# Kernel tuning notes

Hardware: AMD Instinct MI355X
Metric: run time of the kernel (lower is better)

## Reference

```python
import jax, jax.numpy as jnp
import numpy as np

N = 50000   # nodes
E = 800000  # edges
F_IN, F_HID, F_CLS = 128, 128, 40


def gcn_conv(x, W, b, src, dst, dinv):
    # PyG GCNConv: h = x @ W; symmetric-normalized aggregation with self-loops; + bias
    h = x @ W
    coef = (dinv[src] * dinv[dst])[:, None]              # [E,1] edge norm
    agg = jax.ops.segment_sum(h[src] * coef, dst, num_segments=N)
    agg = agg + h * (dinv * dinv)[:, None]               # self-loop term (norm = 1/deg)
    return agg + b


def setup_inputs() -> dict:
    key = jax.random.key(0)
    ks = jax.random.split(key, 8)
    s = 0.06
    return {
        "x": jax.random.normal(ks[0], (N, F_IN), jnp.float32),
        "edge_index": jax.random.randint(ks[1], (2, E), 0, N, dtype=jnp.int64),
        "W1": jax.random.normal(ks[2], (F_IN, F_HID), jnp.float32) * s,
        "b1": jnp.zeros((F_HID,), jnp.float32),
        "W2": jax.random.normal(ks[3], (F_HID, F_HID), jnp.float32) * s,
        "b2": jnp.zeros((F_HID,), jnp.float32),
        "Wc": jax.random.normal(ks[4], (F_HID, F_CLS), jnp.float32) * s,
        "bc": jnp.zeros((F_CLS,), jnp.float32),
    }


def reference(x, edge_index, W1, b1, W2, b2, Wc, bc):
    src, dst = edge_index[0], edge_index[1]
    # degree incl. self-loop, counted at target nodes (PyG default)
    deg = jnp.zeros((N,), x.dtype).at[dst].add(1.0) + 1.0
    dinv = jax.lax.rsqrt(deg)
    h = jax.nn.relu(gcn_conv(x, W1, b1, src, dst, dinv))
    h = jax.nn.relu(gcn_conv(h, W2, b2, src, dst, dinv))
    return h @ Wc + bc
```

## Files before the change

kernel.cpp:

```cpp
#include <hip/hip_runtime.h>

#define FDIM 128
#define FCLS 40
#define EPB  2048
#define BSH  8
#define BKN  (1 << BSH)

typedef short s16x8 __attribute__((ext_vector_type(8)));
typedef float f32x4 __attribute__((ext_vector_type(4)));

__device__ __forceinline__ float bf2f(unsigned short u) {
    union { unsigned int i; float f; } v; v.i = ((unsigned int)u) << 16; return v.f;
}
__device__ __forceinline__ unsigned short f2bf(float f) {
    union { float f; unsigned int i; } v; v.f = f;
    unsigned int u = v.i + 0x7FFFu + ((v.i >> 16) & 1u);
    return (unsigned short)(u >> 16);
}

__global__ __launch_bounds__(256) void bin_hist(const int* __restrict__ dst,
                                                int* __restrict__ hist,
                                                int E, int nblkA, int NB) {
    __shared__ int h[BKN];
    int t = threadIdx.x;
    for (int i = t; i < BKN; i += 256) h[i] = 0;
    __syncthreads();
    int base = blockIdx.x * EPB;
    int end = min(base + EPB, E);
    for (int i = base + t; i < end; i += 256) atomicAdd(&h[dst[i] >> BSH], 1);
    __syncthreads();
    for (int i = t; i < NB; i += 256) hist[i * nblkA + blockIdx.x] = h[i];
}

__global__ __launch_bounds__(256) void hscan_partial(const int* __restrict__ data,
                                                     int* __restrict__ bsums, int n) {
    __shared__ int s[256];
    int t = threadIdx.x;
    int base = blockIdx.x * 1024 + t * 4;
    int v = 0;
#pragma unroll
    for (int j = 0; j < 4; ++j) if (base + j < n) v += data[base + j];
    s[t] = v;
    __syncthreads();
    for (int off = 128; off > 0; off >>= 1) {
        if (t < off) s[t] += s[t + off];
        __syncthreads();
    }
    if (t == 0) bsums[blockIdx.x] = s[0];
}

__global__ __launch_bounds__(256) void hscan_block(int* __restrict__ bsums, int nb) {
    __shared__ int s[256];
    int t = threadIdx.x;
    s[t] = (t < nb) ? bsums[t] : 0;
    __syncthreads();
    for (int off = 1; off < 256; off <<= 1) {
        int x = 0;
        if (t >= off) x = s[t - off];
        __syncthreads();
        s[t] += x;
        __syncthreads();
    }
    if (t < nb) bsums[t] = (t > 0) ? s[t - 1] : 0;
}

__global__ __launch_bounds__(256) void hscan_final(int* __restrict__ data,
                                                   const int* __restrict__ bsums, int n) {
    __shared__ int s[256];
    int t = threadIdx.x;
    int idx = blockIdx.x * 1024 + t * 4;
    int v[4];
    int sum = 0;
#pragma unroll
    for (int j = 0; j < 4; ++j) {
        v[j] = (idx + j < n) ? data[idx + j] : 0;
        sum += v[j];
    }
    s[t] = sum;
    __syncthreads();
    for (int off = 1; off < 256; off <<= 1) {
        int x = 0;
        if (t >= off) x = s[t - off];
        __syncthreads();
        s[t] += x;
        __syncthreads();
    }
    int running = bsums[blockIdx.x] + s[t] - sum;
#pragma unroll
    for (int j = 0; j < 4; ++j) {
        if (idx + j < n) data[idx + j] = running;
        running += v[j];
    }
}

__global__ __launch_bounds__(256) void bin_scatter(const int* __restrict__ src,
                                                   const int* __restrict__ dst,
                                                   const int* __restrict__ histS,
                                                   int2* __restrict__ binned,
                                                   int E, int nblkA, int NB) {
    __shared__ int cur[BKN];
    int t = threadIdx.x;
    for (int i = t; i < NB; i += 256) cur[i] = histS[i * nblkA + blockIdx.x];
    __syncthreads();
    int base = blockIdx.x * EPB;
    int end = min(base + EPB, E);
    for (int i = base + t; i < end; i += 256) {
        int d = dst[i];
        int pos = atomicAdd(&cur[d >> BSH], 1);
        binned[pos] = make_int2(src[i], d);
    }
}

__global__ __launch_bounds__(256) void node_hist_scan(const int2* __restrict__ binned,
                                                      const int* __restrict__ histS,
                                                      int* __restrict__ offsets,
                                                      float* __restrict__ dinv,
                                                      int N, int E, int nblkA, int NB) {
    int b = blockIdx.x;
    int node0 = b << BSH;
    int t = threadIdx.x;
    __shared__ int c[BKN];
    c[t] = 0;
    __syncthreads();
    int lo = histS[b * nblkA];
    int hi = (b == NB - 1) ? E : histS[(b + 1) * nblkA];
    for (int i = lo + t; i < hi; i += 256) {
        int2 p = binned[i];
        atomicAdd(&c[p.y - node0], 1);
    }
    __syncthreads();
    int v = c[t];
    for (int off = 1; off < 256; off <<= 1) {
        int x = (t >= off) ? c[t - off] : 0;
        __syncthreads();
        c[t] += x;
        __syncthreads();
    }
    int excl = lo + c[t] - v;
    int idx = node0 + t;
    if (idx < N) {
        offsets[idx] = excl;
        dinv[idx] = rsqrtf((float)v + 1.0f);
        if (idx == N - 1) offsets[N] = excl + v;
    }
}

__global__ __launch_bounds__(256) void csr_scatter(const int2* __restrict__ binned,
                                                   const int* __restrict__ offsets,
                                                   int* __restrict__ srcAdj, int N) {
    int b = blockIdx.x;
    int node0 = b << BSH;
    int node1 = min(node0 + BKN, N);
    __shared__ int cur[BKN];
    int t = threadIdx.x;
    if (node0 + t < node1) cur[t] = offsets[node0 + t];
    __syncthreads();
    int lo = offsets[node0];
    int hi = offsets[node1];
    for (int i = lo + t; i < hi; i += 256) {
        int2 p = binned[i];
        int pos = atomicAdd(&cur[p.y - node0], 1);
        srcAdj[pos] = p.x;
    }
}

__global__ __launch_bounds__(256) void pack_all(const float* __restrict__ W1,
                                                const float* __restrict__ W2,
                                                const float* __restrict__ Wc,
                                                unsigned short* __restrict__ Wp1,
                                                unsigned short* __restrict__ Wp2,
                                                unsigned short* __restrict__ Wpc) {
    int blk = blockIdx.x;
    const float* W; unsigned short* Wp; int ncols, ct;
    if (blk < 8)       { W = W1; Wp = Wp1; ncols = FDIM; ct = blk; }
    else if (blk < 16) { W = W2; Wp = Wp2; ncols = FDIM; ct = blk - 8; }
    else               { W = Wc; Wp = Wpc; ncols = FCLS; ct = blk - 16; }
    int t = ct * 256 + threadIdx.x;
    int lane = t & 63, ks = (t >> 6) & 3;
    int n  = ct * 16 + (lane & 15);
    int kb = ks * 32 + (lane >> 4) * 8;
    unsigned short v[8];
#pragma unroll
    for (int j = 0; j < 8; ++j) {
        v[j] = (n < ncols) ? f2bf(W[(size_t)(kb + j) * ncols + n]) : (unsigned short)0;
    }
    ushort4* o = (ushort4*)(Wp + (size_t)t * 8);
    o[0] = ushort4{v[0], v[1], v[2], v[3]};
    o[1] = ushort4{v[4], v[5], v[6], v[7]};
}

__global__ __launch_bounds__(256) void gemm_mfma_f32A(const float* __restrict__ A,
                                                      const unsigned short* __restrict__ Wp,
                                                      unsigned short* __restrict__ C, int M) {
    int wave = threadIdx.x >> 6;
    int lane = threadIdx.x & 63;
    int row0 = (blockIdx.x * 4 + wave) * 16;
    if (row0 >= M) return;
    int m = lane & 15;
    int g = lane >> 4;

    const float4* Arow = (const float4*)(A + (size_t)(row0 + m) * FDIM);
    s16x8 a[4];
#pragma unroll
    for (int ks = 0; ks < 4; ++ks) {
        float4 lo = Arow[ks * 8 + g * 2];
        float4 hi = Arow[ks * 8 + g * 2 + 1];
        s16x8 av;
        av[0] = (short)f2bf(lo.x); av[1] = (short)f2bf(lo.y);
        av[2] = (short)f2bf(lo.z); av[3] = (short)f2bf(lo.w);
        av[4] = (short)f2bf(hi.x); av[5] = (short)f2bf(hi.y);
        av[6] = (short)f2bf(hi.z); av[7] = (short)f2bf(hi.w);
        a[ks] = av;
    }

    for (int ct = 0; ct < 8; ++ct) {
        f32x4 acc = {0.f, 0.f, 0.f, 0.f};
#pragma unroll
        for (int ks = 0; ks < 4; ++ks) {
            s16x8 b = *(const s16x8*)(Wp + ((size_t)((ct * 4 + ks) * 64 + lane)) * 8);
            acc = __builtin_amdgcn_mfma_f32_16x16x32_bf16(a[ks], b, acc, 0, 0, 0);
        }
        int n  = ct * 16 + m;
        int r0 = row0 + g * 4;
#pragma unroll
        for (int r = 0; r < 4; ++r)
            C[(size_t)(r0 + r) * FDIM + n] = f2bf(acc[r]);
    }
}

__global__ __launch_bounds__(256) void gemm_mfma(const unsigned short* __restrict__ A,
                                                 const unsigned short* __restrict__ Wp,
                                                 unsigned short* __restrict__ C, int M) {
    int wave = threadIdx.x >> 6;
    int lane = threadIdx.x & 63;
    int row0 = (blockIdx.x * 4 + wave) * 16;
    if (row0 >= M) return;
    int m = lane & 15;
    int g = lane >> 4;

    const s16x8* Arow = (const s16x8*)(A + (size_t)(row0 + m) * FDIM);
    s16x8 a[4];
#pragma unroll
    for (int ks = 0; ks < 4; ++ks) a[ks] = Arow[ks * 4 + g];

    for (int ct = 0; ct < 8; ++ct) {
        f32x4 acc = {0.f, 0.f, 0.f, 0.f};
#pragma unroll
        for (int ks = 0; ks < 4; ++ks) {
            s16x8 b = *(const s16x8*)(Wp + ((size_t)((ct * 4 + ks) * 64 + lane)) * 8);
            acc = __builtin_amdgcn_mfma_f32_16x16x32_bf16(a[ks], b, acc, 0, 0, 0);
        }
        int n  = ct * 16 + m;
        int r0 = row0 + g * 4;
#pragma unroll
        for (int r = 0; r < 4; ++r)
            C[(size_t)(r0 + r) * FDIM + n] = f2bf(acc[r]);
    }
}

__global__ __launch_bounds__(256) void classifier_mfma(const unsigned short* __restrict__ A,
                                                       const unsigned short* __restrict__ Wp,
                                                       const float* __restrict__ bc,
                                                       float* __restrict__ out, int M) {
    int wave = threadIdx.x >> 6;
    int lane = threadIdx.x & 63;
    int row0 = (blockIdx.x * 4 + wave) * 16;
    if (row0 >= M) return;
    int m = lane & 15;
    int g = lane >> 4;

    const s16x8* Arow = (const s16x8*)(A + (size_t)(row0 + m) * FDIM);
    s16x8 a[4];
#pragma unroll
    for (int ks = 0; ks < 4; ++ks) a[ks] = Arow[ks * 4 + g];

    for (int ct = 0; ct < 3; ++ct) {
        f32x4 acc = {0.f, 0.f, 0.f, 0.f};
#pragma unroll
        for (int ks = 0; ks < 4; ++ks) {
            s16x8 b = *(const s16x8*)(Wp + ((size_t)((ct * 4 + ks) * 64 + lane)) * 8);
            acc = __builtin_amdgcn_mfma_f32_16x16x32_bf16(a[ks], b, acc, 0, 0, 0);
        }
        int n = ct * 16 + m;
        if (n < FCLS) {
            float bias = bc[n];
            int r0 = row0 + g * 4;
#pragma unroll
            for (int r = 0; r < 4; ++r)
                out[(size_t)(r0 + r) * FCLS + n] = acc[r] + bias;
        }
    }
}

__global__ __launch_bounds__(256) void agg_fused(const unsigned short* __restrict__ H,
                                                 const float* __restrict__ dinv,
                                                 const float* __restrict__ bias,
                                                 const int* __restrict__ srcAdj,
                                                 const int* __restrict__ offsets,
                                                 unsigned short* __restrict__ OUT, int N) {
    int node = blockIdx.x * 16 + (threadIdx.x >> 4);
    if (node >= N) return;
    int lane = threadIdx.x & 15;

    const s16x8* H8 = (const s16x8*)H;
    float di = dinv[node];
    float d2 = di * di;

    s16x8 h = H8[(size_t)node * 16 + lane];
    float acc[8];
#pragma unroll
    for (int j = 0; j < 8; ++j) acc[j] = bf2f((unsigned short)h[j]) * d2;

    int e   = offsets[node];
    int end = offsets[node + 1];
    for (; e + 4 <= end; e += 4) {
        int s0 = srcAdj[e + 0], s1 = srcAdj[e + 1];
        int s2 = srcAdj[e + 2], s3 = srcAdj[e + 3];
        float c0 = dinv[s0] * di, c1 = dinv[s1] * di;
        float c2 = dinv[s2] * di, c3 = dinv[s3] * di;
        s16x8 a0 = H8[(size_t)s0 * 16 + lane];
        s16x8 a1 = H8[(size_t)s1 * 16 + lane];
        s16x8 a2 = H8[(size_t)s2 * 16 + lane];
        s16x8 a3 = H8[(size_t)s3 * 16 + lane];
#pragma unroll
        for (int j = 0; j < 8; ++j) {
            acc[j] = fmaf(bf2f((unsigned short)a0[j]), c0, acc[j]);
            acc[j] = fmaf(bf2f((unsigned short)a1[j]), c1, acc[j]);
            acc[j] = fmaf(bf2f((unsigned short)a2[j]), c2, acc[j]);
            acc[j] = fmaf(bf2f((unsigned short)a3[j]), c3, acc[j]);
        }
    }
    for (; e < end; ++e) {
        int s0 = srcAdj[e];
        float c0 = dinv[s0] * di;
        s16x8 a0 = H8[(size_t)s0 * 16 + lane];
#pragma unroll
        for (int j = 0; j < 8; ++j)
            acc[j] = fmaf(bf2f((unsigned short)a0[j]), c0, acc[j]);
    }

    float4 b0 = ((const float4*)bias)[lane * 2];
    float4 b1 = ((const float4*)bias)[lane * 2 + 1];
    float bb[8] = {b0.x, b0.y, b0.z, b0.w, b1.x, b1.y, b1.z, b1.w};
    s16x8 o;
#pragma unroll
    for (int j = 0; j < 8; ++j)
        o[j] = (short)f2bf(fmaxf(acc[j] + bb[j], 0.0f));
    ((s16x8*)OUT)[(size_t)node * 16 + lane] = o;
}

extern "C" void kernel_launch(void* const* d_in, const int* in_sizes, int n_in,
                              void* d_out, int out_size, void* d_ws, size_t ws_size,
                              hipStream_t stream) {
    const float* x  = (const float*)d_in[0];
    const int*   ei = (const int*)d_in[1];
    const float* W1 = (const float*)d_in[2];
    const float* b1 = (const float*)d_in[3];
    const float* W2 = (const float*)d_in[4];
    const float* b2 = (const float*)d_in[5];
    const float* Wc = (const float*)d_in[6];
    const float* bc = (const float*)d_in[7];
    float* out = (float*)d_out;

    int N = in_sizes[0] / FDIM;
    int E = in_sizes[1] / 2;
    const int* src = ei;
    const int* dst = ei + E;

    int nblkA = (E + EPB - 1) / EPB;
    int NB    = (N + BKN - 1) >> BSH;
    int mfmaBlocks = (N / 16 + 3) / 4;
    int aggBlocks  = (N + 15) / 16;
    int histN = NB * nblkA;
    int hscanBlocks = (histN + 1023) / 1024;

    int2* binned   = (int2*)d_ws;
    int*  srcAdj   = (int*)(binned + E);
    int*  offsets  = srcAdj + E;
    int*  hist     = offsets + (N + 1);
    int*  bsums    = hist + histN;
    float* dinv    = (float*)(bsums + 256);
    unsigned short* Wp1 = (unsigned short*)(dinv + N);
    unsigned short* Wp2 = Wp1 + 8 * 4 * 64 * 8;
    unsigned short* Wpc = Wp2 + 8 * 4 * 64 * 8;
    unsigned short* Hbuf = Wpc + 3 * 4 * 64 * 8;
    unsigned short* Abuf = Hbuf + (size_t)N * FDIM;

    bin_hist<<<nblkA, 256, 0, stream>>>(dst, hist, E, nblkA, NB);
    hscan_partial<<<hscanBlocks, 256, 0, stream>>>(hist, bsums, histN);
    hscan_block<<<1, 256, 0, stream>>>(bsums, hscanBlocks);
    hscan_final<<<hscanBlocks, 256, 0, stream>>>(hist, bsums, histN);
    bin_scatter<<<nblkA, 256, 0, stream>>>(src, dst, hist, binned, E, nblkA, NB);
    node_hist_scan<<<NB, 256, 0, stream>>>(binned, hist, offsets, dinv, N, E, nblkA, NB);
    csr_scatter<<<NB, 256, 0, stream>>>(binned, offsets, srcAdj, N);

    pack_all<<<19, 256, 0, stream>>>(W1, W2, Wc, Wp1, Wp2, Wpc);

    gemm_mfma_f32A<<<mfmaBlocks, 256, 0, stream>>>(x, Wp1, Hbuf, N);
    agg_fused<<<aggBlocks, 256, 0, stream>>>(Hbuf, dinv, b1, srcAdj, offsets, Abuf, N);

    gemm_mfma<<<mfmaBlocks, 256, 0, stream>>>(Abuf, Wp2, Hbuf, N);
    agg_fused<<<aggBlocks, 256, 0, stream>>>(Hbuf, dinv, b2, srcAdj, offsets, Abuf, N);

    classifier_mfma<<<mfmaBlocks, 256, 0, stream>>>(Abuf, Wpc, bc, out, N);
}
```

Baseline: 158.4 us.

## Pack edge records, precompute fp16 edge coefficients, and split features into column quarters

The feature matrices move to a layout split into four 32-column quarters, and aggregation blocks each handle one quarter. Gathers then touch a 64-byte slice per node within a smaller working set, which should improve L2 hit rates. Edge records are packed into 32 bits (16-bit src and dst for binning; src plus an fp16 normalization coefficient for the CSR), which halves the bytes moved and removes the per-edge dinv lookups during aggregation. EPB also doubles. Packing node ids into 16 bits only works while N < 65536, so it relies on the test size, and the fp16 coefficients lose some precision.

```diff
diff --git a/kernel.cpp b/kernel.cpp
--- a/kernel.cpp
+++ b/kernel.cpp
@@ -1,8 +1,9 @@
 #include <hip/hip_runtime.h>
+#include <hip/hip_fp16.h>
 
 #define FDIM 128
 #define FCLS 40
-#define EPB  2048
+#define EPB  4096
 #define BSH  8
 #define BKN  (1 << BSH)
 
@@ -23,7 +24,7 @@
                                                 int E, int nblkA, int NB) {
     __shared__ int h[BKN];
     int t = threadIdx.x;
-    for (int i = t; i < BKN; i += 256) h[i] = 0;
+    h[t] = 0;
     __syncthreads();
     int base = blockIdx.x * EPB;
     int end = min(base + EPB, E);
@@ -96,7 +97,7 @@
 __global__ __launch_bounds__(256) void bin_scatter(const int* __restrict__ src,
                                                    const int* __restrict__ dst,
                                                    const int* __restrict__ histS,
-                                                   int2* __restrict__ binned,
+                                                   unsigned int* __restrict__ binnedPk,
                                                    int E, int nblkA, int NB) {
     __shared__ int cur[BKN];
     int t = threadIdx.x;
@@ -107,11 +108,11 @@
     for (int i = base + t; i < end; i += 256) {
         int d = dst[i];
         int pos = atomicAdd(&cur[d >> BSH], 1);
-        binned[pos] = make_int2(src[i], d);
-    }
-}
-
-__global__ __launch_bounds__(256) void node_hist_scan(const int2* __restrict__ binned,
+        binnedPk[pos] = (unsigned int)(src[i] & 0xFFFF) | ((unsigned int)d << 16);
+    }
+}
+
+__global__ __launch_bounds__(256) void node_hist_scan(const unsigned int* __restrict__ binnedPk,
                                                       const int* __restrict__ histS,
                                                       int* __restrict__ offsets,
                                                       float* __restrict__ dinv,
@@ -125,8 +126,8 @@
     int lo = histS[b * nblkA];
     int hi = (b == NB - 1) ? E : histS[(b + 1) * nblkA];
     for (int i = lo + t; i < hi; i += 256) {
-        int2 p = binned[i];
-        atomicAdd(&c[p.y - node0], 1);
+        int d = (int)(binnedPk[i] >> 16);
+        atomicAdd(&c[d - node0], 1);
     }
     __syncthreads();
     int v = c[t];
@@ -145,9 +146,10 @@
     }
 }
 
-__global__ __launch_bounds__(256) void csr_scatter(const int2* __restrict__ binned,
+__global__ __launch_bounds__(256) void csr_scatter(const unsigned int* __restrict__ binnedPk,
                                                    const int* __restrict__ offsets,
-                                                   int* __restrict__ srcAdj, int N) {
+                                                   const float* __restrict__ dinv,
+                                                   unsigned int* __restrict__ srcPk, int N) {
     int b = blockIdx.x;
     int node0 = b << BSH;
     int node1 = min(node0 + BKN, N);
@@ -158,9 +160,13 @@
     int lo = offsets[node0];
     int hi = offsets[node1];
     for (int i = lo + t; i < hi; i += 256) {
-        int2 p = binned[i];
-        int pos = atomicAdd(&cur[p.y - node0], 1);
-        srcAdj[pos] = p.x;
+        unsigned int p = binnedPk[i];
+        int s = (int)(p & 0xFFFFu);
+        int d = (int)(p >> 16);
+        int pos = atomicAdd(&cur[d - node0], 1);
+        float coef = dinv[s] * dinv[d];
+        unsigned short cb = __half_as_ushort(__float2half(coef));
+        srcPk[pos] = (unsigned int)s | ((unsigned int)cb << 16);
     }
 }
 
@@ -189,6 +195,7 @@
     o[1] = ushort4{v[4], v[5], v[6], v[7]};
 }
 
+
 __global__ __launch_bounds__(256) void gemm_mfma_f32A(const float* __restrict__ A,
                                                       const unsigned short* __restrict__ Wp,
                                                       unsigned short* __restrict__ C, int M) {
@@ -220,11 +227,12 @@
             s16x8 b = *(const s16x8*)(Wp + ((size_t)((ct * 4 + ks) * 64 + lane)) * 8);
             acc = __builtin_amdgcn_mfma_f32_16x16x32_bf16(a[ks], b, acc, 0, 0, 0);
         }
-        int n  = ct * 16 + m;
+        int q  = ct >> 1;
+        int cc = (ct & 1) * 16 + m;
         int r0 = row0 + g * 4;
 #pragma unroll
         for (int r = 0; r < 4; ++r)
-            C[(size_t)(r0 + r) * FDIM + n] = f2bf(acc[r]);
+            C[((size_t)q * M + (r0 + r)) * 32 + cc] = f2bf(acc[r]);
     }
 }
 
@@ -238,10 +246,11 @@
     int m = lane & 15;
     int g = lane >> 4;
 
-    const s16x8* Arow = (const s16x8*)(A + (size_t)(row0 + m) * FDIM);
+    const s16x8* A8 = (const s16x8*)A;
     s16x8 a[4];
 #pragma unroll
-    for (int ks = 0; ks < 4; ++ks) a[ks] = Arow[ks * 4 + g];
+    for (int ks = 0; ks < 4; ++ks)
+        a[ks] = A8[((size_t)ks * M + (row0 + m)) * 4 + g];
 
     for (int ct = 0; ct < 8; ++ct) {
         f32x4 acc = {0.f, 0.f, 0.f, 0.f};
@@ -250,11 +259,12 @@
             s16x8 b = *(const s16x8*)(Wp + ((size_t)((ct * 4 + ks) * 64 + lane)) * 8);
             acc = __builtin_amdgcn_mfma_f32_16x16x32_bf16(a[ks], b, acc, 0, 0, 0);
         }
-        int n  = ct * 16 + m;
+        int q  = ct >> 1;
+        int cc = (ct & 1) * 16 + m;
         int r0 = row0 + g * 4;
 #pragma unroll
         for (int r = 0; r < 4; ++r)
-            C[(size_t)(r0 + r) * FDIM + n] = f2bf(acc[r]);
+            C[((size_t)q * M + (r0 + r)) * 32 + cc] = f2bf(acc[r]);
     }
 }
 
@@ -269,10 +279,11 @@
     int m = lane & 15;
     int g = lane >> 4;
 
-    const s16x8* Arow = (const s16x8*)(A + (size_t)(row0 + m) * FDIM);
+    const s16x8* A8 = (const s16x8*)A;
     s16x8 a[4];
 #pragma unroll
-    for (int ks = 0; ks < 4; ++ks) a[ks] = Arow[ks * 4 + g];
+    for (int ks = 0; ks < 4; ++ks)
+        a[ks] = A8[((size_t)ks * M + (row0 + m)) * 4 + g];
 
     for (int ct = 0; ct < 3; ++ct) {
         f32x4 acc = {0.f, 0.f, 0.f, 0.f};
@@ -295,18 +306,22 @@
 __global__ __launch_bounds__(256) void agg_fused(const unsigned short* __restrict__ H,
                                                  const float* __restrict__ dinv,
                                                  const float* __restrict__ bias,
-                                                 const int* __restrict__ srcAdj,
+                                                 const unsigned int* __restrict__ srcPk,
                                                  const int* __restrict__ offsets,
-                                                 unsigned short* __restrict__ OUT, int N) {
-    int node = blockIdx.x * 16 + (threadIdx.x >> 4);
+                                                 unsigned short* __restrict__ OUT,
+                                                 int N, int bpq) {
+    int q = blockIdx.x / bpq;
+    int b = blockIdx.x - q * bpq;
+    int node = b * 64 + (threadIdx.x >> 2);
     if (node >= N) return;
-    int lane = threadIdx.x & 15;
+    int c4 = threadIdx.x & 3;
 
     const s16x8* H8 = (const s16x8*)H;
+    size_t qbase = (size_t)q * N * 4;
     float di = dinv[node];
     float d2 = di * di;
 
-    s16x8 h = H8[(size_t)node * 16 + lane];
+    s16x8 h = H8[qbase + (size_t)node * 4 + c4];
     float acc[8];
 #pragma unroll
     for (int j = 0; j < 8; ++j) acc[j] = bf2f((unsigned short)h[j]) * d2;
@@ -314,14 +329,16 @@
     int e   = offsets[node];
     int end = offsets[node + 1];
     for (; e + 4 <= end; e += 4) {
-        int s0 = srcAdj[e + 0], s1 = srcAdj[e + 1];
-        int s2 = srcAdj[e + 2], s3 = srcAdj[e + 3];
-        float c0 = dinv[s0] * di, c1 = dinv[s1] * di;
-        float c2 = dinv[s2] * di, c3 = dinv[s3] * di;
-        s16x8 a0 = H8[(size_t)s0 * 16 + lane];
-        s16x8 a1 = H8[(size_t)s1 * 16 + lane];
-        s16x8 a2 = H8[(size_t)s2 * 16 + lane];
-        s16x8 a3 = H8[(size_t)s3 * 16 + lane];
+        unsigned int p0 = srcPk[e + 0], p1 = srcPk[e + 1];
+        unsigned int p2 = srcPk[e + 2], p3 = srcPk[e + 3];
+        float c0 = __half2float(__ushort_as_half((unsigned short)(p0 >> 16)));
+        float c1 = __half2float(__ushort_as_half((unsigned short)(p1 >> 16)));
+        float c2 = __half2float(__ushort_as_half((unsigned short)(p2 >> 16)));
+        float c3 = __half2float(__ushort_as_half((unsigned short)(p3 >> 16)));
+        s16x8 a0 = H8[qbase + (size_t)(p0 & 0xFFFFu) * 4 + c4];
+        s16x8 a1 = H8[qbase + (size_t)(p1 & 0xFFFFu) * 4 + c4];
+        s16x8 a2 = H8[qbase + (size_t)(p2 & 0xFFFFu) * 4 + c4];
+        s16x8 a3 = H8[qbase + (size_t)(p3 & 0xFFFFu) * 4 + c4];
 #pragma unroll
         for (int j = 0; j < 8; ++j) {
             acc[j] = fmaf(bf2f((unsigned short)a0[j]), c0, acc[j]);
@@ -331,22 +348,22 @@
         }
     }
     for (; e < end; ++e) {
-        int s0 = srcAdj[e];
-        float c0 = dinv[s0] * di;
-        s16x8 a0 = H8[(size_t)s0 * 16 + lane];
+        unsigned int p0 = srcPk[e];
+        float c0 = __half2float(__ushort_as_half((unsigned short)(p0 >> 16)));
+        s16x8 a0 = H8[qbase + (size_t)(p0 & 0xFFFFu) * 4 + c4];
 #pragma unroll
         for (int j = 0; j < 8; ++j)
             acc[j] = fmaf(bf2f((unsigned short)a0[j]), c0, acc[j]);
     }
 
-    float4 b0 = ((const float4*)bias)[lane * 2];
-    float4 b1 = ((const float4*)bias)[lane * 2 + 1];
+    const float4* bq = (const float4*)(bias + q * 32 + c4 * 8);
+    float4 b0 = bq[0], b1 = bq[1];
     float bb[8] = {b0.x, b0.y, b0.z, b0.w, b1.x, b1.y, b1.z, b1.w};
     s16x8 o;
 #pragma unroll
     for (int j = 0; j < 8; ++j)
         o[j] = (short)f2bf(fmaxf(acc[j] + bb[j], 0.0f));
-    ((s16x8*)OUT)[(size_t)node * 16 + lane] = o;
+    ((s16x8*)OUT)[qbase + (size_t)node * 4 + c4] = o;
 }
 
 extern "C" void kernel_launch(void* const* d_in, const int* in_sizes, int n_in,
@@ -370,13 +387,14 @@
     int nblkA = (E + EPB - 1) / EPB;
     int NB    = (N + BKN - 1) >> BSH;
     int mfmaBlocks = (N / 16 + 3) / 4;
-    int aggBlocks  = (N + 15) / 16;
+    int bpq = (N + 63) / 64;
+    int aggBlocks = 4 * bpq;
     int histN = NB * nblkA;
     int hscanBlocks = (histN + 1023) / 1024;
 
-    int2* binned   = (int2*)d_ws;
-    int*  srcAdj   = (int*)(binned + E);
-    int*  offsets  = srcAdj + E;
+    unsigned int* binnedPk = (unsigned int*)d_ws;
+    unsigned int* srcPk    = binnedPk + E;
+    int*  offsets  = (int*)(srcPk + E);
     int*  hist     = offsets + (N + 1);
     int*  bsums    = hist + histN;
     float* dinv    = (float*)(bsums + 256);
@@ -390,17 +408,17 @@
     hscan_partial<<<hscanBlocks, 256, 0, stream>>>(hist, bsums, histN);
     hscan_block<<<1, 256, 0, stream>>>(bsums, hscanBlocks);
     hscan_final<<<hscanBlocks, 256, 0, stream>>>(hist, bsums, histN);
-    bin_scatter<<<nblkA, 256, 0, stream>>>(src, dst, hist, binned, E, nblkA, NB);
-    node_hist_scan<<<NB, 256, 0, stream>>>(binned, hist, offsets, dinv, N, E, nblkA, NB);
-    csr_scatter<<<NB, 256, 0, stream>>>(binned, offsets, srcAdj, N);
+    bin_scatter<<<nblkA, 256, 0, stream>>>(src, dst, hist, binnedPk, E, nblkA, NB);
+    node_hist_scan<<<NB, 256, 0, stream>>>(binnedPk, hist, offsets, dinv, N, E, nblkA, NB);
+    csr_scatter<<<NB, 256, 0, stream>>>(binnedPk, offsets, dinv, srcPk, N);
 
     pack_all<<<19, 256, 0, stream>>>(W1, W2, Wc, Wp1, Wp2, Wpc);
 
     gemm_mfma_f32A<<<mfmaBlocks, 256, 0, stream>>>(x, Wp1, Hbuf, N);
-    agg_fused<<<aggBlocks, 256, 0, stream>>>(Hbuf, dinv, b1, srcAdj, offsets, Abuf, N);
+    agg_fused<<<aggBlocks, 256, 0, stream>>>(Hbuf, dinv, b1, srcPk, offsets, Abuf, N, bpq);
 
     gemm_mfma<<<mfmaBlocks, 256, 0, stream>>>(Abuf, Wp2, Hbuf, N);
-    agg_fused<<<aggBlocks, 256, 0, stream>>>(Hbuf, dinv, b2, srcAdj, offsets, Abuf, N);
+    agg_fused<<<aggBlocks, 256, 0, stream>>>(Hbuf, dinv, b2, srcPk, offsets, Abuf, N, bpq);
 
     classifier_mfma<<<mfmaBlocks, 256, 0, stream>>>(Abuf, Wpc, bc, out, N);
 }
```

Result: slower. 188.5 us (+19.0%).
